# Optimization experiments

Hardware: AMD Instinct MI355X
Metric: run time of the kernel (lower is better)

The kernel has to match this reference:

```python
import jax, jax.numpy as jnp
import numpy as np

N = 300      # grid resolution
R = 48       # rank (components per mode)
B = 1048576  # number of query points


def setup_inputs() -> dict:
    key = jax.random.key(0)
    k1, k2, k3 = jax.random.split(key, 3)
    # 3D points in normalized grid_sample coordinates [-1, 1]
    coords = jax.random.uniform(k1, (B, 3), jnp.float32, -1.0, 1.0)
    # learned params (kaiming-uniform-like scale; exact init irrelevant for math)
    matrices = jax.random.normal(k2, (3, R, N, N), jnp.float32) * 0.1
    vectors = jax.random.normal(k3, (3, R, N, 1), jnp.float32) * 0.1
    return {"coords": coords, "matrices": matrices, "vectors": vectors}


def _bilinear_sample(img, x, y):
    """Faithful torch F.grid_sample(mode='bilinear', padding_mode='zeros',
    align_corners=False) for a single image.
    img: (C, H, W); x, y: (B,) in [-1, 1] (x indexes W, y indexes H).
    Returns (C, B).
    """
    C, H, W = img.shape
    # unnormalize (align_corners=False)
    ix = (x + 1.0) * (W * 0.5) - 0.5
    iy = (y + 1.0) * (H * 0.5) - 0.5
    ix0f = jnp.floor(ix)
    iy0f = jnp.floor(iy)
    wx = ix - ix0f  # frac weights
    wy = iy - iy0f
    ix0 = ix0f.astype(jnp.int32)
    iy0 = iy0f.astype(jnp.int32)
    ix1 = ix0 + 1
    iy1 = iy0 + 1

    def gather(iy_, ix_):
        valid = (ix_ >= 0) & (ix_ < W) & (iy_ >= 0) & (iy_ < H)
        v = img[:, jnp.clip(iy_, 0, H - 1), jnp.clip(ix_, 0, W - 1)]  # (C, B)
        return jnp.where(valid, v, 0.0)

    return (gather(iy0, ix0) * ((1.0 - wy) * (1.0 - wx))
            + gather(iy0, ix1) * ((1.0 - wy) * wx)
            + gather(iy1, ix0) * (wy * (1.0 - wx))
            + gather(iy1, ix1) * (wy * wx))


def reference(coords, matrices, vectors):
    b = coords.shape[0]
    # mat grid: x = input[:, (i+1)%3], y = input[:, (i+2)%3]
    x_mat = jnp.stack([coords[:, 1], coords[:, 2], coords[:, 0]], axis=0)  # (3, B)
    y_mat = jnp.stack([coords[:, 2], coords[:, 0], coords[:, 1]], axis=0)  # (3, B)
    # vec grid: x = input[:, i], y = 0
    x_vec = coords.T                      # (3, B)
    y_vec = jnp.zeros_like(x_vec)
    mat_out = jax.vmap(_bilinear_sample)(matrices, x_mat, y_mat)  # (3, R, B)
    vec_out = jax.vmap(_bilinear_sample)(vectors, x_vec, y_vec)   # (3, R, B)
    prod = mat_out * vec_out                                      # (3, R, B)
    # torch: (3,R,B,1).permute(2,0,1,3).view(B, 3*R)
    return jnp.transpose(prod, (2, 0, 1)).reshape(b, 3 * R)
```

## Files before the change

### kernel.cpp

```cpp
#include <hip/hip_runtime.h>
#include <hip/hip_fp16.h>

constexpr int N_ = 300;
constexpr int R_ = 48;
constexpr int B_ = 1048576;
constexpr int NCHUNK = 8;
constexpr int NLBIN = 24;
constexpr int SUBS = 8;
constexpr int NCELL = NLBIN * SUBS;
constexpr int CAP = 16640;
constexpr int CNT_STRIDE = 32;
constexpr int OVF_CAP = 32768;
constexpr int BPB = (CAP * 6 + 255) / 256;
constexpr int VPX = 3 * SUBS * BPB;
constexpr unsigned GATHER_BLOCKS = 8 * VPX;

constexpr size_t OFF_MT   = 0;
constexpr size_t OFF_VSUM = 25920000;
constexpr size_t OFF_CNT  = 25920640;
constexpr size_t OFF_OCUR = 25945216;
constexpr size_t OFF_OVF  = 25945344;
constexpr size_t OFF_REC  = 26076416;

typedef float f32x4 __attribute__((ext_vector_type(4)));
union H8 { float4 f4; __half2 h2[4]; };

__global__ __launch_bounds__(256) void k_prep(const float* __restrict__ mat,
                                              const float* __restrict__ vec,
                                              __half2* __restrict__ mt2,
                                              float* __restrict__ vsum,
                                              int* __restrict__ counts,
                                              int* __restrict__ ocur) {
    if (blockIdx.x == 900) {
        int t = threadIdx.x;
        if (t < 3 * R_) vsum[t] = 0.5f * (vec[t * N_ + 149] + vec[t * N_ + 150]);
        for (int k = t; k < NCELL * CNT_STRIDE; k += 256) counts[k] = 0;
        if (t == 255) *ocur = 0;
        return;
    }
    __shared__ float tile[R_][N_ + 1];
    int i = blockIdx.x / N_;
    int y = blockIdx.x - i * N_;
    const float* src = mat + ((size_t)i * R_ * N_ + y) * N_;
    for (int idx = threadIdx.x; idx < R_ * N_; idx += 256) {
        int r = idx / N_;
        int x = idx - r * N_;
        tile[r][x] = src[(size_t)r * N_ * N_ + x];
    }
    __syncthreads();
    __half2* dst = mt2 + (size_t)(i * N_ + y) * N_ * (R_ / 2);
    for (int idx = threadIdx.x; idx < N_ * (R_ / 2); idx += 256) {
        int x  = idx / (R_ / 2);
        int jj = idx - x * (R_ / 2);
        dst[idx] = __floats2half2_rn(tile[2 * jj][x], tile[2 * jj + 1][x]);
    }
}

struct BW { float w00, w01, w10, w11; int o00, o01, o10, o11; };
__device__ inline BW bilin_ix(float ix, float iy) {
    float ix0f = floorf(ix), iy0f = floorf(iy);
    float wx = ix - ix0f, wy = iy - iy0f;
    int ix0 = (int)ix0f, iy0 = (int)iy0f;
    int ix1 = ix0 + 1, iy1 = iy0 + 1;
    BW r;
    r.w00 = (1.0f - wy) * (1.0f - wx);
    r.w01 = (1.0f - wy) * wx;
    r.w10 = wy * (1.0f - wx);
    r.w11 = wy * wx;
    bool bx0 = (unsigned)ix0 < (unsigned)N_;
    bool bx1 = (unsigned)ix1 < (unsigned)N_;
    bool by0 = (unsigned)iy0 < (unsigned)N_;
    bool by1 = (unsigned)iy1 < (unsigned)N_;
    if (!(bx0 && by0)) r.w00 = 0.0f;
    if (!(bx1 && by0)) r.w01 = 0.0f;
    if (!(bx0 && by1)) r.w10 = 0.0f;
    if (!(bx1 && by1)) r.w11 = 0.0f;
    int cx0 = min(max(ix0, 0), N_ - 1), cx1 = min(max(ix1, 0), N_ - 1);
    int cy0 = min(max(iy0, 0), N_ - 1), cy1 = min(max(iy1, 0), N_ - 1);
    r.o00 = (cy0 * N_ + cx0) * R_;
    r.o01 = (cy0 * N_ + cx1) * R_;
    r.o10 = (cy1 * N_ + cx0) * R_;
    r.o11 = (cy1 * N_ + cx1) * R_;
    return r;
}

__device__ inline void plane_xy(int plane, float c0, float c1, float c2,
                                float& xc, float& yc, float& cc) {
    if (plane == 0)      { xc = c1; yc = c2; cc = c0; }
    else if (plane == 1) { xc = c2; yc = c0; cc = c1; }
    else                 { xc = c0; yc = c1; cc = c2; }
}

__global__ __launch_bounds__(256) void k_scatter(const float* __restrict__ coords,
                                                 int* __restrict__ counts,
                                                 unsigned* __restrict__ recs,
                                                 int* __restrict__ ocur,
                                                 unsigned* __restrict__ ovf) {
    __shared__ int lcnt[NLBIN];
    __shared__ int lbase[NLBIN];
    int tid = threadIdx.x;
    if (tid < NLBIN) lcnt[tid] = 0;
    __syncthreads();

    int b = blockIdx.x * 256 + tid;
    int sub = blockIdx.x & 7;
    float c0 = coords[3 * b], c1 = coords[3 * b + 1], c2 = coords[3 * b + 2];

    int lbin[3], lpos[3];
#pragma unroll
    for (int plane = 0; plane < 3; ++plane) {
        float xc, yc, cc;
        plane_xy(plane, c0, c1, c2, xc, yc, cc);
        float iy = (yc + 1.0f) * 150.0f - 0.5f;
        int row = (int)floorf(iy) + 1;
        int chunk = row * 8 / 301;
        lbin[plane] = plane * NCHUNK + chunk;
        lpos[plane] = atomicAdd(&lcnt[lbin[plane]], 1);
    }
    __syncthreads();
    if (tid < NLBIN) {
        int cell = tid * SUBS + sub;
        lbase[tid] = atomicAdd(&counts[cell * CNT_STRIDE], lcnt[tid]);
    }
    __syncthreads();
#pragma unroll
    for (int plane = 0; plane < 3; ++plane) {
        int pos = lbase[lbin[plane]] + lpos[plane];
        int cell = lbin[plane] * SUBS + sub;
        if (pos < CAP) {
            recs[(size_t)cell * CAP + pos] = (unsigned)b;
        } else {
            int o = atomicAdd(ocur, 1);
            if (o < OVF_CAP) ovf[o] = (unsigned)b | ((unsigned)plane << 20);
        }
    }
}

__global__ __launch_bounds__(256) void k_gather(const float* __restrict__ coords,
                                                const int* __restrict__ counts,
                                                const unsigned* __restrict__ recs,
                                                const __half* __restrict__ M,
                                                const float* __restrict__ vsum,
                                                float* __restrict__ out) {
    unsigned bid = blockIdx.x;
    unsigned chunk = bid & 7;
    unsigned v = bid >> 3;
    unsigned plane = v / (SUBS * BPB);
    unsigned r0 = v - plane * (SUBS * BPB);
    unsigned sub = r0 / BPB;
    unsigned lb  = r0 - sub * BPB;
    unsigned cell = (plane * NCHUNK + chunk) * SUBS + sub;
    int cnt = min(counts[cell * CNT_STRIDE], CAP);
    unsigned g = lb * 256 + threadIdx.x;
    unsigned slot = g / 6;
    unsigned j = g - slot * 6;
    if ((int)slot >= cnt) return;

    int b = (int)recs[(size_t)cell * CAP + slot];

    float c0 = coords[3 * b], c1 = coords[3 * b + 1], c2 = coords[3 * b + 2];
    float xc, yc, cc;
    plane_xy((int)plane, c0, c1, c2, xc, yc, cc);

    float ix = (xc + 1.0f) * 150.0f - 0.5f;
    float iy = (yc + 1.0f) * 150.0f - 0.5f;
    BW w = bilin_ix(ix, iy);
    const __half* Mi = M + (size_t)plane * N_ * N_ * R_;
    int co = 8 * j;

    H8 u00, u01, u10, u11;
    u00.f4 = *reinterpret_cast<const float4*>(Mi + w.o00 + co);
    u01.f4 = *reinterpret_cast<const float4*>(Mi + w.o01 + co);
    u10.f4 = *reinterpret_cast<const float4*>(Mi + w.o10 + co);
    u11.f4 = *reinterpret_cast<const float4*>(Mi + w.o11 + co);

    float vw = 1.0f - 0.5f * fabsf(cc);
    const float4* vs4 = reinterpret_cast<const float4*>(vsum + plane * R_ + co);
    float4 vv0 = vs4[0];
    float4 vv1 = vs4[1];

    float r[8];
#pragma unroll
    for (int k = 0; k < 4; ++k) {
        float2 a00 = __half22float2(u00.h2[k]);
        float2 a01 = __half22float2(u01.h2[k]);
        float2 a10 = __half22float2(u10.h2[k]);
        float2 a11 = __half22float2(u11.h2[k]);
        r[2 * k]     = fmaf(a00.x, w.w00, fmaf(a01.x, w.w01, fmaf(a10.x, w.w10, a11.x * w.w11)));
        r[2 * k + 1] = fmaf(a00.y, w.w00, fmaf(a01.y, w.w01, fmaf(a10.y, w.w10, a11.y * w.w11)));
    }

    f32x4 s0, s1;
    s0.x = r[0] * (vv0.x * vw); s0.y = r[1] * (vv0.y * vw);
    s0.z = r[2] * (vv0.z * vw); s0.w = r[3] * (vv0.w * vw);
    s1.x = r[4] * (vv1.x * vw); s1.y = r[5] * (vv1.y * vw);
    s1.z = r[6] * (vv1.z * vw); s1.w = r[7] * (vv1.w * vw);

    float* outp = out + (size_t)b * 144 + plane * 48 + co;
    __builtin_nontemporal_store(s0, reinterpret_cast<f32x4*>(outp));
    __builtin_nontemporal_store(s1, reinterpret_cast<f32x4*>(outp) + 1);
}

__global__ __launch_bounds__(256) void k_overflow(const float* __restrict__ coords,
                                                  const int* __restrict__ ocur,
                                                  const unsigned* __restrict__ ovf,
                                                  const __half* __restrict__ M,
                                                  const float* __restrict__ vsum,
                                                  float* __restrict__ out) {
    int cnt = min(*ocur, OVF_CAP);
    for (int t = blockIdx.x * 256 + threadIdx.x; t < cnt; t += gridDim.x * 256) {
        unsigned rec = ovf[t];
        int b = (int)(rec & 0xFFFFF);
        int plane = (int)(rec >> 20);
        float c0 = coords[3 * b], c1 = coords[3 * b + 1], c2 = coords[3 * b + 2];
        float xc, yc, cc;
        plane_xy(plane, c0, c1, c2, xc, yc, cc);
        float ix = (xc + 1.0f) * 150.0f - 0.5f;
        float iy = (yc + 1.0f) * 150.0f - 0.5f;
        BW w = bilin_ix(ix, iy);
        float vw = 1.0f - 0.5f * fabsf(cc);
        const __half* Mi = M + (size_t)plane * N_ * N_ * R_;
        for (int j = 0; j < 6; ++j) {
            H8 u00, u01, u10, u11;
            u00.f4 = *reinterpret_cast<const float4*>(Mi + w.o00 + 8 * j);
            u01.f4 = *reinterpret_cast<const float4*>(Mi + w.o01 + 8 * j);
            u10.f4 = *reinterpret_cast<const float4*>(Mi + w.o10 + 8 * j);
            u11.f4 = *reinterpret_cast<const float4*>(Mi + w.o11 + 8 * j);
            for (int k = 0; k < 4; ++k) {
                float2 a00 = __half22float2(u00.h2[k]);
                float2 a01 = __half22float2(u01.h2[k]);
                float2 a10 = __half22float2(u10.h2[k]);
                float2 a11 = __half22float2(u11.h2[k]);
                float r0 = fmaf(a00.x, w.w00, fmaf(a01.x, w.w01, fmaf(a10.x, w.w10, a11.x * w.w11)));
                float r1 = fmaf(a00.y, w.w00, fmaf(a01.y, w.w01, fmaf(a10.y, w.w10, a11.y * w.w11)));
                out[(size_t)b * 144 + plane * 48 + 8 * j + 2 * k]     = r0 * (vsum[plane * R_ + 8 * j + 2 * k] * vw);
                out[(size_t)b * 144 + plane * 48 + 8 * j + 2 * k + 1] = r1 * (vsum[plane * R_ + 8 * j + 2 * k + 1] * vw);
            }
        }
    }
}

extern "C" void kernel_launch(void* const* d_in, const int* in_sizes, int n_in,
                              void* d_out, int out_size, void* d_ws, size_t ws_size,
                              hipStream_t stream) {
    const float* coords   = (const float*)d_in[0];
    const float* matrices = (const float*)d_in[1];
    const float* vectors  = (const float*)d_in[2];
    float* out = (float*)d_out;

    __half*   mt     = (__half*)((char*)d_ws + OFF_MT);
    float*    vsum   = (float*)((char*)d_ws + OFF_VSUM);
    int*      counts = (int*)((char*)d_ws + OFF_CNT);
    int*      ocur   = (int*)((char*)d_ws + OFF_OCUR);
    unsigned* ovf    = (unsigned*)((char*)d_ws + OFF_OVF);
    unsigned* recs   = (unsigned*)((char*)d_ws + OFF_REC);

    hipLaunchKernelGGL(k_prep, dim3(901), dim3(256), 0, stream,
                       matrices, vectors, (__half2*)mt, vsum, counts, ocur);
    hipLaunchKernelGGL(k_scatter, dim3(B_ / 256), dim3(256), 0, stream,
                       coords, counts, recs, ocur, ovf);
    hipLaunchKernelGGL(k_gather, dim3(GATHER_BLOCKS), dim3(256), 0, stream,
                       coords, counts, recs, mt, vsum, out);
    hipLaunchKernelGGL(k_overflow, dim3(64), dim3(256), 0, stream,
                       coords, ocur, ovf, mt, vsum, out);
}
```

Measured before the change: 235.5 us.

## Bin points by joint 3D row chunks and gather all planes per point

Points are now binned by a combined 4x4x4 row-chunk key over all three coordinates instead of per-plane row chunks. Each gather thread therefore processes all three planes for one point, sharing the record and coords loads and writing the point's contiguous 144-float output row. The overflow path is folded into the gather kernel as extra blocks, which removes one launch. The trade-off is that each bin now spans a wider slice of every plane, which may lower L2 locality for the matrix gathers, and the smaller per-cell capacity may push more points onto the slower overflow path.

```diff
diff --git a/kernel.cpp b/kernel.cpp
--- a/kernel.cpp
+++ b/kernel.cpp
@@ -4,23 +4,24 @@
 constexpr int N_ = 300;
 constexpr int R_ = 48;
 constexpr int B_ = 1048576;
-constexpr int NCHUNK = 8;
-constexpr int NLBIN = 24;
+constexpr int NBIN3 = 64;
 constexpr int SUBS = 8;
-constexpr int NCELL = NLBIN * SUBS;
-constexpr int CAP = 16640;
+constexpr int NCELL = NBIN3 * SUBS;
+constexpr int CAP = 2304;
 constexpr int CNT_STRIDE = 32;
-constexpr int OVF_CAP = 32768;
-constexpr int BPB = (CAP * 6 + 255) / 256;
-constexpr int VPX = 3 * SUBS * BPB;
-constexpr unsigned GATHER_BLOCKS = 8 * VPX;
+constexpr int OVF_CAP = 262144;
+constexpr int BPB = CAP * 6 / 256;
+constexpr unsigned GB_MAIN = NCELL * BPB;
+constexpr unsigned XCHUNK = GB_MAIN / 8;
+constexpr unsigned OVF_BLOCKS = 64;
+constexpr unsigned GRID_GATHER = GB_MAIN + OVF_BLOCKS;
 
 constexpr size_t OFF_MT   = 0;
 constexpr size_t OFF_VSUM = 25920000;
 constexpr size_t OFF_CNT  = 25920640;
-constexpr size_t OFF_OCUR = 25945216;
-constexpr size_t OFF_OVF  = 25945344;
-constexpr size_t OFF_REC  = 26076416;
+constexpr size_t OFF_OCUR = 25986176;
+constexpr size_t OFF_OVF  = 25986304;
+constexpr size_t OFF_REC  = 27034880;
 
 typedef float f32x4 __attribute__((ext_vector_type(4)));
 union H8 { float4 f4; __half2 h2[4]; };
@@ -35,7 +36,7 @@
         int t = threadIdx.x;
         if (t < 3 * R_) vsum[t] = 0.5f * (vec[t * N_ + 149] + vec[t * N_ + 150]);
         for (int k = t; k < NCELL * CNT_STRIDE; k += 256) counts[k] = 0;
-        if (t == 255) *ocur = 0;
+        if (t == 0) *ocur = 0;
         return;
     }
     __shared__ float tile[R_][N_ + 1];
@@ -91,77 +92,12 @@
     else                 { xc = c0; yc = c1; cc = c2; }
 }
 
-__global__ __launch_bounds__(256) void k_scatter(const float* __restrict__ coords,
-                                                 int* __restrict__ counts,
-                                                 unsigned* __restrict__ recs,
-                                                 int* __restrict__ ocur,
-                                                 unsigned* __restrict__ ovf) {
-    __shared__ int lcnt[NLBIN];
-    __shared__ int lbase[NLBIN];
-    int tid = threadIdx.x;
-    if (tid < NLBIN) lcnt[tid] = 0;
-    __syncthreads();
-
-    int b = blockIdx.x * 256 + tid;
-    int sub = blockIdx.x & 7;
-    float c0 = coords[3 * b], c1 = coords[3 * b + 1], c2 = coords[3 * b + 2];
-
-    int lbin[3], lpos[3];
-#pragma unroll
-    for (int plane = 0; plane < 3; ++plane) {
-        float xc, yc, cc;
-        plane_xy(plane, c0, c1, c2, xc, yc, cc);
-        float iy = (yc + 1.0f) * 150.0f - 0.5f;
-        int row = (int)floorf(iy) + 1;
-        int chunk = row * 8 / 301;
-        lbin[plane] = plane * NCHUNK + chunk;
-        lpos[plane] = atomicAdd(&lcnt[lbin[plane]], 1);
-    }
-    __syncthreads();
-    if (tid < NLBIN) {
-        int cell = tid * SUBS + sub;
-        lbase[tid] = atomicAdd(&counts[cell * CNT_STRIDE], lcnt[tid]);
-    }
-    __syncthreads();
-#pragma unroll
-    for (int plane = 0; plane < 3; ++plane) {
-        int pos = lbase[lbin[plane]] + lpos[plane];
-        int cell = lbin[plane] * SUBS + sub;
-        if (pos < CAP) {
-            recs[(size_t)cell * CAP + pos] = (unsigned)b;
-        } else {
-            int o = atomicAdd(ocur, 1);
-            if (o < OVF_CAP) ovf[o] = (unsigned)b | ((unsigned)plane << 20);
-        }
-    }
-}
-
-__global__ __launch_bounds__(256) void k_gather(const float* __restrict__ coords,
-                                                const int* __restrict__ counts,
-                                                const unsigned* __restrict__ recs,
-                                                const __half* __restrict__ M,
-                                                const float* __restrict__ vsum,
-                                                float* __restrict__ out) {
-    unsigned bid = blockIdx.x;
-    unsigned chunk = bid & 7;
-    unsigned v = bid >> 3;
-    unsigned plane = v / (SUBS * BPB);
-    unsigned r0 = v - plane * (SUBS * BPB);
-    unsigned sub = r0 / BPB;
-    unsigned lb  = r0 - sub * BPB;
-    unsigned cell = (plane * NCHUNK + chunk) * SUBS + sub;
-    int cnt = min(counts[cell * CNT_STRIDE], CAP);
-    unsigned g = lb * 256 + threadIdx.x;
-    unsigned slot = g / 6;
-    unsigned j = g - slot * 6;
-    if ((int)slot >= cnt) return;
-
-    int b = (int)recs[(size_t)cell * CAP + slot];
-
-    float c0 = coords[3 * b], c1 = coords[3 * b + 1], c2 = coords[3 * b + 2];
+__device__ inline void sample8(int plane, int j, int b, float c0, float c1, float c2,
+                               const __half* __restrict__ M,
+                               const float* __restrict__ vsum,
+                               float* __restrict__ out) {
     float xc, yc, cc;
-    plane_xy((int)plane, c0, c1, c2, xc, yc, cc);
-
+    plane_xy(plane, c0, c1, c2, xc, yc, cc);
     float ix = (xc + 1.0f) * 150.0f - 0.5f;
     float iy = (yc + 1.0f) * 150.0f - 0.5f;
     BW w = bilin_ix(ix, iy);
@@ -201,43 +137,79 @@
     __builtin_nontemporal_store(s1, reinterpret_cast<f32x4*>(outp) + 1);
 }
 
-__global__ __launch_bounds__(256) void k_overflow(const float* __restrict__ coords,
-                                                  const int* __restrict__ ocur,
-                                                  const unsigned* __restrict__ ovf,
-                                                  const __half* __restrict__ M,
-                                                  const float* __restrict__ vsum,
-                                                  float* __restrict__ out) {
-    int cnt = min(*ocur, OVF_CAP);
-    for (int t = blockIdx.x * 256 + threadIdx.x; t < cnt; t += gridDim.x * 256) {
-        unsigned rec = ovf[t];
-        int b = (int)(rec & 0xFFFFF);
-        int plane = (int)(rec >> 20);
-        float c0 = coords[3 * b], c1 = coords[3 * b + 1], c2 = coords[3 * b + 2];
-        float xc, yc, cc;
-        plane_xy(plane, c0, c1, c2, xc, yc, cc);
-        float ix = (xc + 1.0f) * 150.0f - 0.5f;
-        float iy = (yc + 1.0f) * 150.0f - 0.5f;
-        BW w = bilin_ix(ix, iy);
-        float vw = 1.0f - 0.5f * fabsf(cc);
-        const __half* Mi = M + (size_t)plane * N_ * N_ * R_;
-        for (int j = 0; j < 6; ++j) {
-            H8 u00, u01, u10, u11;
-            u00.f4 = *reinterpret_cast<const float4*>(Mi + w.o00 + 8 * j);
-            u01.f4 = *reinterpret_cast<const float4*>(Mi + w.o01 + 8 * j);
-            u10.f4 = *reinterpret_cast<const float4*>(Mi + w.o10 + 8 * j);
-            u11.f4 = *reinterpret_cast<const float4*>(Mi + w.o11 + 8 * j);
-            for (int k = 0; k < 4; ++k) {
-                float2 a00 = __half22float2(u00.h2[k]);
-                float2 a01 = __half22float2(u01.h2[k]);
-                float2 a10 = __half22float2(u10.h2[k]);
-                float2 a11 = __half22float2(u11.h2[k]);
-                float r0 = fmaf(a00.x, w.w00, fmaf(a01.x, w.w01, fmaf(a10.x, w.w10, a11.x * w.w11)));
-                float r1 = fmaf(a00.y, w.w00, fmaf(a01.y, w.w01, fmaf(a10.y, w.w10, a11.y * w.w11)));
-                out[(size_t)b * 144 + plane * 48 + 8 * j + 2 * k]     = r0 * (vsum[plane * R_ + 8 * j + 2 * k] * vw);
-                out[(size_t)b * 144 + plane * 48 + 8 * j + 2 * k + 1] = r1 * (vsum[plane * R_ + 8 * j + 2 * k + 1] * vw);
-            }
+__device__ inline int row_chunk(float c) {
+    float i = (c + 1.0f) * 150.0f - 0.5f;
+    int row = (int)floorf(i) + 1;
+    return (row * 4) / 301;
+}
+
+__global__ __launch_bounds__(256) void k_scatter(const float* __restrict__ coords,
+                                                 int* __restrict__ counts,
+                                                 unsigned* __restrict__ recs,
+                                                 int* __restrict__ ocur,
+                                                 unsigned* __restrict__ ovf) {
+    __shared__ int lcnt[NBIN3];
+    __shared__ int lbase[NBIN3];
+    int tid = threadIdx.x;
+    if (tid < NBIN3) lcnt[tid] = 0;
+    __syncthreads();
+
+    int b = blockIdx.x * 256 + tid;
+    int sub = blockIdx.x & 7;
+    float c0 = coords[3 * b], c1 = coords[3 * b + 1], c2 = coords[3 * b + 2];
+    int bin = row_chunk(c0) * 16 + row_chunk(c1) * 4 + row_chunk(c2);
+    int lpos = atomicAdd(&lcnt[bin], 1);
+    __syncthreads();
+    if (tid < NBIN3) {
+        int cell = tid * SUBS + sub;
+        lbase[tid] = atomicAdd(&counts[cell * CNT_STRIDE], lcnt[tid]);
+    }
+    __syncthreads();
+    int pos = lbase[bin] + lpos;
+    int cell = bin * SUBS + sub;
+    if (pos < CAP) {
+        recs[(size_t)cell * CAP + pos] = (unsigned)b;
+    } else {
+        int o = atomicAdd(ocur, 1);
+        if (o < OVF_CAP) ovf[o] = (unsigned)b;
+    }
+}
+
+__global__ __launch_bounds__(256) void k_gather(const float* __restrict__ coords,
+                                                const int* __restrict__ counts,
+                                                const unsigned* __restrict__ recs,
+                                                const int* __restrict__ ocur,
+                                                const unsigned* __restrict__ ovf,
+                                                const __half* __restrict__ M,
+                                                const float* __restrict__ vsum,
+                                                float* __restrict__ out) {
+    unsigned bid = blockIdx.x;
+    if (bid >= GB_MAIN) {
+        int cnt = min(*ocur, OVF_CAP);
+        for (int t = (bid - GB_MAIN) * 256 + threadIdx.x; t < cnt; t += OVF_BLOCKS * 256) {
+            int b = (int)ovf[t];
+            float c0 = coords[3 * b], c1 = coords[3 * b + 1], c2 = coords[3 * b + 2];
+#pragma unroll
+            for (int p = 0; p < 3; ++p)
+                for (int j = 0; j < 6; ++j)
+                    sample8(p, j, b, c0, c1, c2, M, vsum, out);
         }
-    }
+        return;
+    }
+    unsigned vbid = (bid & 7) * XCHUNK + (bid >> 3);
+    unsigned cell = vbid / BPB;
+    unsigned lb   = vbid - cell * BPB;
+    unsigned g = lb * 256 + threadIdx.x;
+    unsigned slot = g / 6;
+    unsigned j = g - slot * 6;
+    int cnt = min(counts[cell * CNT_STRIDE], CAP);
+    if ((int)slot >= cnt) return;
+
+    int b = (int)recs[(size_t)cell * CAP + slot];
+    float c0 = coords[3 * b], c1 = coords[3 * b + 1], c2 = coords[3 * b + 2];
+#pragma unroll
+    for (int p = 0; p < 3; ++p)
+        sample8(p, (int)j, b, c0, c1, c2, M, vsum, out);
 }
 
 extern "C" void kernel_launch(void* const* d_in, const int* in_sizes, int n_in,
@@ -259,8 +231,6 @@
                        matrices, vectors, (__half2*)mt, vsum, counts, ocur);
     hipLaunchKernelGGL(k_scatter, dim3(B_ / 256), dim3(256), 0, stream,
                        coords, counts, recs, ocur, ovf);
-    hipLaunchKernelGGL(k_gather, dim3(GATHER_BLOCKS), dim3(256), 0, stream,
-                       coords, counts, recs, mt, vsum, out);
-    hipLaunchKernelGGL(k_overflow, dim3(64), dim3(256), 0, stream,
-                       coords, ocur, ovf, mt, vsum, out);
-}
+    hipLaunchKernelGGL(k_gather, dim3(GRID_GATHER), dim3(256), 0, stream,
+                       coords, counts, recs, ocur, ovf, mt, vsum, out);
+}
```

After: 229.4 us. 1.03x faster.
